# Optimization experiments

Measured on AMD Instinct MI355X. Metric: run time of the kernel, lower is better.

Reference implementation:

```python
import jax, jax.numpy as jnp
import numpy as np

N, NFEAT, NHID, NCLASS, NHEADS = 4096, 512, 64, 40, 8
ALPHA = 0.2  # LeakyReLU negative slope
NEG_BIG = -9e15


def _xavier(key, shape, gain=1.414):
    fan_in, fan_out = shape[0], shape[1]
    bound = gain * np.sqrt(6.0 / (fan_in + fan_out))
    return jax.random.uniform(key, shape, jnp.float32, -bound, bound)


def setup_inputs() -> dict:
    key = jax.random.key(0)
    ks = jax.random.split(key, 6)
    x = jax.random.normal(ks[0], (N, NFEAT), jnp.float32)
    adj = jax.random.randint(ks[1], (N, N), 0, 2).astype(jnp.float32)
    # per-head params of the 8 input GAT layers
    Ws = _xavier(ks[2], (NHEADS, NFEAT, NHID))          # stacked W: [H, F, D]
    a_s = _xavier(ks[3], (NHEADS, 2 * NHID, 1))[..., 0]  # [H, 2D]
    # output GAT layer (concat=False)
    W_out = _xavier(ks[4], (NHID * NHEADS, NCLASS))
    a_out = _xavier(ks[5], (2 * NCLASS, 1))[..., 0]      # [2C]
    return {"x": x, "adj": adj, "Ws": Ws, "a_s": a_s, "W_out": W_out, "a_out": a_out}


def _gat_layer(inp, adj_mask, W, a, concat):
    # h = inp @ W : [N, D]
    h = inp @ W
    D = h.shape[1]
    a1, a2 = a[:D], a[D:]
    # e[i,j] = leakyrelu(a . [h_i, h_j]) = leakyrelu(h_i.a1 + h_j.a2)
    # (same math as the N*N*2D concat in the original, without materializing it)
    f1 = h @ a1  # [N]
    f2 = h @ a2  # [N]
    e = jax.nn.leaky_relu(f1[:, None] + f2[None, :], negative_slope=ALPHA)
    att = jax.nn.softmax(jnp.where(adj_mask, e, NEG_BIG), axis=1)
    h_prime = att @ h  # [N, D]
    return jax.nn.elu(h_prime) if concat else h_prime


def reference(x, adj, Ws, a_s, W_out, a_out):
    adj_mask = adj > 0
    # 8 attention heads over the input features (eval mode: dropout is identity)
    heads = jax.vmap(lambda W, a: _gat_layer(x, adj_mask, W, a, True))(Ws, a_s)  # [H, N, D]
    x2 = jnp.transpose(heads, (1, 0, 2)).reshape(N, NHEADS * NHID)  # concat along feature dim
    out = _gat_layer(x2, adj_mask, W_out, a_out, False)  # [N, C]
    out = jax.nn.elu(out)
    return jax.nn.log_softmax(out, axis=1)
```

## Files before the change

kernel.cpp:

```cpp
#include <hip/hip_runtime.h>
#include <hip/hip_bf16.h>
#include <stdint.h>

#define NN 4096
#define NF 512
#define NH 64
#define NCLS 40
#define NHEADS 8
#define LOG2E 1.4426950408889634f

typedef __attribute__((ext_vector_type(8))) short bh8;
typedef __attribute__((ext_vector_type(4))) float f32x4;

__device__ __forceinline__ unsigned short f2bu(float f) {
    union { float f; unsigned u; } v; v.f = f;
    unsigned r = (v.u + 0x7FFFu + ((v.u >> 16) & 1u)) >> 16;
    return (unsigned short)r;
}
__device__ __forceinline__ float lrelu(float x) { return fmaxf(x, 0.2f * x); }
__device__ __forceinline__ float elu1(float x) { return x > 0.f ? x : expm1f(x); }
__device__ __forceinline__ float exp2fast(float x) {
    float r; asm("v_exp_f32 %0, %1" : "=v"(r) : "v"(x)); return r;
}
__device__ __forceinline__ unsigned fenc(float f) {
    unsigned u = __builtin_bit_cast(unsigned, f);
    return ((int)u < 0) ? ~u : (u | 0x80000000u);
}
__device__ __forceinline__ float fdec(unsigned k) {
    unsigned u = (k & 0x80000000u) ? (k ^ 0x80000000u) : ~k;
    return __builtin_bit_cast(float, u);
}
__device__ __forceinline__ int sbfe1(unsigned v, int off) {
#if __has_builtin(__builtin_amdgcn_sbfe)
    return __builtin_amdgcn_sbfe((int)v, off, 1);
#else
    return ((int)(v << (31 - off))) >> 31;
#endif
}
__device__ __forceinline__ float bmask(float p, unsigned mdw, int bit) {
    return __builtin_bit_cast(float,
        __builtin_bit_cast(unsigned, p) & (unsigned)sbfe1(mdw, bit));
}
__device__ __forceinline__ unsigned pack2(float x, float y) {
    unsigned ux = __builtin_bit_cast(unsigned, x), uy = __builtin_bit_cast(unsigned, y);
    ux += 0x7FFFu + ((ux >> 16) & 1u);
    uy += 0x7FFFu + ((uy >> 16) & 1u);
    return __builtin_amdgcn_perm(uy, ux, 0x07060302u);
}

__global__ __launch_bounds__(256) void prep_all_k(const float* __restrict__ x,
                                                  const float* __restrict__ adj,
                                                  const float* __restrict__ Ws,
                                                  const float* __restrict__ Wo,
                                                  unsigned short* __restrict__ xb,
                                                  unsigned short* __restrict__ WT,
                                                  unsigned short* __restrict__ WoT,
                                                  unsigned char* __restrict__ adjp,
                                                  unsigned* __restrict__ FM1u,
                                                  unsigned* __restrict__ FM2u) {
    const int bid = blockIdx.x, tid = threadIdx.x;
    if (bid < 8192) {
        __shared__ unsigned char sm[4][64];
        const int i = bid >> 1, half = bid & 1;
        const float* rp = adj + (size_t)i * NN + half * 2048 + tid * 8;
        float4 v0 = ((const float4*)rp)[0];
        float4 v1 = ((const float4*)rp)[1];
        unsigned b = (v0.x > 0.f ? 1u : 0u) | (v0.y > 0.f ? 2u : 0u) |
                     (v0.z > 0.f ? 4u : 0u) | (v0.w > 0.f ? 8u : 0u) |
                     (v1.x > 0.f ? 16u : 0u) | (v1.y > 0.f ? 32u : 0u) |
                     (v1.z > 0.f ? 64u : 0u) | (v1.w > 0.f ? 128u : 0u);
        sm[tid & 3][tid >> 2] = (unsigned char)b;
        __syncthreads();
        if (tid < 64) {
            int gp = tid >> 4, word = tid & 15;
            unsigned d = *(const unsigned*)&sm[gp][word * 4];
            *(unsigned*)(adjp + ((size_t)i * 4 + gp) * 128 + half * 64 + word * 4) = d;
        }
    } else if (bid < 10240) {
        if (bid == 8192) {
            if (tid < 8) FM1u[tid] = 0u;
            if (tid == 8) FM2u[0] = 0u;
        }
        int t = (bid - 8192) * 256 + tid;
        float4 v = ((const float4*)x)[t];
        uint2 o; o.x = pack2(v.x, v.y); o.y = pack2(v.z, v.w);
        ((uint2*)xb)[t] = o;
    } else if (bid < 11264) {
        int j = (bid - 10240) * 256 + tid;
        int c = j >> 9, k = j & 511;
        WT[j] = f2bu(Ws[(size_t)(c >> 6) * (NF * NH) + (size_t)k * NH + (c & 63)]);
    } else {
        int j = (bid - 11264) * 256 + tid;
        int c = j >> 9, k = j & 511;
        WoT[j] = f2bu(c < NCLS ? Wo[(size_t)k * NCLS + c] : 0.f);
    }
}

__global__ __launch_bounds__(512) void gemm1_k(const unsigned short* __restrict__ xb,
                                               const unsigned short* __restrict__ WT,
                                               const float* __restrict__ a_s,
                                               unsigned short* __restrict__ Bp1,
                                               float* __restrict__ f1L,
                                               float* __restrict__ f2L,
                                               unsigned* __restrict__ FM1u) {
    __shared__ unsigned short xs[128 * 40];
    __shared__ unsigned short wsm[64 * 40];
    const int tid = threadIdx.x;
    const int w = tid >> 6, lane = tid & 63, r16 = lane & 15, grp = lane >> 4;
    const int i0 = blockIdx.x << 7, h = blockIdx.y, c0 = h << 6;
    const int srow = tid >> 2, sseg = tid & 3;
    const unsigned short* xsrc = xb + (size_t)(i0 + srow) * NF + sseg * 8;
    const unsigned short* wsrc = WT + (size_t)(c0 + (srow & 63)) * NF + sseg * 8;
    f32x4 a0 = {0,0,0,0}, a1 = {0,0,0,0}, a2 = {0,0,0,0}, a3 = {0,0,0,0};
    bh8 rx = *(const bh8*)(xsrc);
    bh8 rw; if (tid < 256) rw = *(const bh8*)(wsrc);
    for (int kb = 0; kb < NF; kb += 32) {
        *(bh8*)(xs + srow * 40 + sseg * 8) = rx;
        if (tid < 256) *(bh8*)(wsm + srow * 40 + sseg * 8) = rw;
        __syncthreads();
        if (kb + 32 < NF) {
            rx = *(const bh8*)(xsrc + kb + 32);
            if (tid < 256) rw = *(const bh8*)(wsrc + kb + 32);
        }
        bh8 af = *(const bh8*)(xs + (w * 16 + r16) * 40 + grp * 8);
        bh8 b0 = *(const bh8*)(wsm + (r16) * 40 + grp * 8);
        bh8 b1 = *(const bh8*)(wsm + (16 + r16) * 40 + grp * 8);
        bh8 b2 = *(const bh8*)(wsm + (32 + r16) * 40 + grp * 8);
        bh8 b3 = *(const bh8*)(wsm + (48 + r16) * 40 + grp * 8);
        a0 = __builtin_amdgcn_mfma_f32_16x16x32_bf16(af, b0, a0, 0, 0, 0);
        a1 = __builtin_amdgcn_mfma_f32_16x16x32_bf16(af, b1, a1, 0, 0, 0);
        a2 = __builtin_amdgcn_mfma_f32_16x16x32_bf16(af, b2, a2, 0, 0, 0);
        a3 = __builtin_amdgcn_mfma_f32_16x16x32_bf16(af, b3, a3, 0, 0, 0);
        __syncthreads();
    }
    const int jt = (i0 >> 5) + (w >> 1);
    const int kg = ((w & 1) << 1) + (grp >> 1);
    const int lanep = kg * 16 + r16;
    const int ebase = (grp & 1) * 4;
    unsigned short* bp = Bp1 + ((size_t)(h * 128 + jt)) * 2048 + lanep * 8 + ebase;
    {
        uint2 v;
        v.x = pack2(a0[0], a0[1]); v.y = pack2(a0[2], a0[3]); *(uint2*)(bp + 0 * 512) = v;
        v.x = pack2(a1[0], a1[1]); v.y = pack2(a1[2], a1[3]); *(uint2*)(bp + 1 * 512) = v;
        v.x = pack2(a2[0], a2[1]); v.y = pack2(a2[2], a2[3]); *(uint2*)(bp + 2 * 512) = v;
        v.x = pack2(a3[0], a3[1]); v.y = pack2(a3[2], a3[3]); *(uint2*)(bp + 3 * 512) = v;
    }
    const float* ap = a_s + h * 128;
    float a1v[4], a2v[4];
#pragma unroll
    for (int n = 0; n < 4; ++n) { a1v[n] = ap[r16 + 16 * n]; a2v[n] = ap[64 + r16 + 16 * n]; }
    float wmax = -3.0e38f;
#pragma unroll
    for (int r = 0; r < 4; ++r) {
        const int orow = i0 + w * 16 + grp * 4 + r;
        float s1 = a0[r] * a1v[0] + a1[r] * a1v[1] + a2[r] * a1v[2] + a3[r] * a1v[3];
        float s2 = a0[r] * a2v[0] + a1[r] * a2v[1] + a2[r] * a2v[2] + a3[r] * a2v[3];
#pragma unroll
        for (int o2 = 1; o2 < 16; o2 <<= 1) { s1 += __shfl_xor(s1, o2); s2 += __shfl_xor(s2, o2); }
        s1 *= LOG2E; s2 *= LOG2E;
        if (r16 == 0) { f1L[h * NN + orow] = s1; f2L[h * NN + orow] = s2; }
        wmax = fmaxf(wmax, s2);
    }
    wmax = fmaxf(wmax, __shfl_xor(wmax, 16));
    wmax = fmaxf(wmax, __shfl_xor(wmax, 32));
    if (lane == 0) atomicMax(&FM1u[h], fenc(wmax));
}

__global__ __launch_bounds__(256) void gemm2_k(const unsigned short* __restrict__ x2b,
                                               const unsigned short* __restrict__ WoT,
                                               const float* __restrict__ a_out,
                                               unsigned short* __restrict__ Bp2,
                                               float* __restrict__ f12L,
                                               float* __restrict__ f22L,
                                               unsigned* __restrict__ FM2u) {
    __shared__ unsigned short xs[64 * 40];
    __shared__ unsigned short wsm[48 * 40];
    const int tid = threadIdx.x;
    const int w = tid >> 6, lane = tid & 63, r16 = lane & 15, grp = lane >> 4;
    const int i0 = blockIdx.x << 6;
    const int srow = tid >> 2, sseg = tid & 3;
    const unsigned short* xsrc = x2b + (size_t)(i0 + srow) * NF + sseg * 8;
    const unsigned short* wsrc = WoT + (size_t)srow * NF + sseg * 8;
    f32x4 a0 = {0,0,0,0}, a1 = {0,0,0,0}, a2 = {0,0,0,0};
    bh8 rx = *(const bh8*)(xsrc);
    bh8 rw; if (tid < 192) rw = *(const bh8*)(wsrc);
    for (int kb = 0; kb < NF; kb += 32) {
        *(bh8*)(xs + srow * 40 + sseg * 8) = rx;
        if (tid < 192) *(bh8*)(wsm + srow * 40 + sseg * 8) = rw;
        __syncthreads();
        if (kb + 32 < NF) {
            rx = *(const bh8*)(xsrc + kb + 32);
            if (tid < 192) rw = *(const bh8*)(wsrc + kb + 32);
        }
        bh8 af = *(const bh8*)(xs + (w * 16 + r16) * 40 + grp * 8);
        bh8 b0 = *(const bh8*)(wsm + (r16) * 40 + grp * 8);
        bh8 b1 = *(const bh8*)(wsm + (16 + r16) * 40 + grp * 8);
        bh8 b2 = *(const bh8*)(wsm + (32 + r16) * 40 + grp * 8);
        a0 = __builtin_amdgcn_mfma_f32_16x16x32_bf16(af, b0, a0, 0, 0, 0);
        a1 = __builtin_amdgcn_mfma_f32_16x16x32_bf16(af, b1, a1, 0, 0, 0);
        a2 = __builtin_amdgcn_mfma_f32_16x16x32_bf16(af, b2, a2, 0, 0, 0);
        __syncthreads();
    }
    const int jt = (i0 >> 5) + (w >> 1);
    const int kg = ((w & 1) << 1) + (grp >> 1);
    const int lanep = kg * 16 + r16;
    const int ebase = (grp & 1) * 4;
    unsigned short* bp = Bp2 + (size_t)jt * 1536 + lanep * 8 + ebase;
    {
        uint2 v;
        v.x = pack2(a0[0], a0[1]); v.y = pack2(a0[2], a0[3]); *(uint2*)(bp + 0 * 512) = v;
        v.x = pack2(a1[0], a1[1]); v.y = pack2(a1[2], a1[3]); *(uint2*)(bp + 1 * 512) = v;
        v.x = pack2(a2[0], a2[1]); v.y = pack2(a2[2], a2[3]); *(uint2*)(bp + 2 * 512) = v;
    }
    float a1v[3], a2v[3];
#pragma unroll
    for (int n = 0; n < 3; ++n) {
        int col = r16 + 16 * n;
        a1v[n] = col < NCLS ? a_out[col] : 0.f;
        a2v[n] = col < NCLS ? a_out[NCLS + col] : 0.f;
    }
    float wmax = -3.0e38f;
#pragma unroll
    for (int r = 0; r < 4; ++r) {
        const int orow = i0 + w * 16 + grp * 4 + r;
        float s1 = a0[r] * a1v[0] + a1[r] * a1v[1] + a2[r] * a1v[2];
        float s2 = a0[r] * a2v[0] + a1[r] * a2v[1] + a2[r] * a2v[2];
#pragma unroll
        for (int o2 = 1; o2 < 16; o2 <<= 1) { s1 += __shfl_xor(s1, o2); s2 += __shfl_xor(s2, o2); }
        s1 *= LOG2E; s2 *= LOG2E;
        if (r16 == 0) { f12L[orow] = s1; f22L[orow] = s2; }
        wmax = fmaxf(wmax, s2);
    }
    wmax = fmaxf(wmax, __shfl_xor(wmax, 16));
    wmax = fmaxf(wmax, __shfl_xor(wmax, 32));
    if (lane == 0) atomicMax(&FM2u[0], fenc(wmax));
}

__global__ __launch_bounds__(512, 6) void attn1_k(const unsigned short* __restrict__ Bp1,
                                                  const unsigned char* __restrict__ adjp,
                                                  const float* __restrict__ f1L,
                                                  const float* __restrict__ f2L,
                                                  const unsigned* __restrict__ FM1u,
                                                  unsigned short* __restrict__ x2b) {
    __shared__ float EFs[8192];
    const int tid = threadIdx.x, w = tid >> 6, lane = tid & 63;
    const int r16 = lane & 15, grp = lane >> 4;
    const int rowg = w & 3, jq = w >> 2;
    const int h = blockIdx.y;
    const int i0 = blockIdx.x * 64;
    const float fm = fdec(FM1u[h]);
    const float* f2p = f2L + h * NN;
    for (int t = 0; t < 8; ++t) {
        int j = tid + t * 512;
        float d = f2p[j] - fm;
        EFs[2 * j] = exp2fast(d);
        EFs[2 * j + 1] = exp2fast(0.2f * d);
    }
    const int irow = i0 + rowg * 16 + r16;
    const float f1v = f1L[h * NN + irow];
    const float mL = lrelu(f1v + fm);
    const float A = exp2fast(f1v + fm - mL);
    const float B = exp2fast(__builtin_fmaf(0.2f, f1v + fm, -mL));
    __syncthreads();
    const int jtbase = jq * 64;
    const unsigned char* adjr = adjp + ((size_t)irow * 4 + grp) * 128 + jtbase;
    const float* efp = EFs + grp * 16;
    const unsigned short* Bbase = Bp1 + (size_t)h * 128 * 2048 + lane * 8;
    f32x4 acc0 = {0,0,0,0}, acc1 = {0,0,0,0}, acc2 = {0,0,0,0}, acc3 = {0,0,0,0}, accd = {0,0,0,0};
    const short ov = (r16 == 0) ? (short)0x3F80 : (short)0;
    bh8 ones;
#pragma unroll
    for (int e = 0; e < 8; ++e) ones[e] = ov;
    bh8 nb0, nb1, nb2, nb3;
#define PREF1(JT) { const unsigned short* Bn = Bbase + (size_t)(JT) * 2048;              \
        nb0 = *(const bh8*)(Bn);        nb1 = *(const bh8*)(Bn + 512);                    \
        nb2 = *(const bh8*)(Bn + 1024); nb3 = *(const bh8*)(Bn + 1536); }
    PREF1(jtbase);
    for (int jt16 = 0; jt16 < 4; ++jt16) {
        const uint4 a4 = *(const uint4*)(adjr + jt16 * 16);
#pragma unroll
        for (int q = 0; q < 4; ++q) {
            const unsigned mdw = (q == 0) ? a4.x : (q == 1) ? a4.y : (q == 2) ? a4.z : a4.w;
#pragma unroll
            for (int u = 0; u < 4; ++u) {
                const int jt = jtbase + jt16 * 16 + q * 4 + u;
                bh8 b0 = nb0, b1 = nb1, b2 = nb2, b3 = nb3;
                PREF1(jt + 1);
                const float* e4 = efp + jt * 64;
                float4 ea = *(const float4*)(e4);
                float4 eb = *(const float4*)(e4 + 4);
                float4 ec = *(const float4*)(e4 + 8);
                float4 ed = *(const float4*)(e4 + 12);
                const int bb = u * 8;
                union { bh8 v; unsigned u32[4]; } pk;
                {
                    float p0 = bmask(fmaxf(A * ea.x, B * ea.y), mdw, bb + 0);
                    float p1 = bmask(fmaxf(A * ea.z, B * ea.w), mdw, bb + 1);
                    pk.u32[0] = __builtin_amdgcn_perm(__builtin_bit_cast(unsigned, p1),
                                                      __builtin_bit_cast(unsigned, p0), 0x07060302u);
                    float p2 = bmask(fmaxf(A * eb.x, B * eb.y), mdw, bb + 2);
                    float p3 = bmask(fmaxf(A * eb.z, B * eb.w), mdw, bb + 3);
                    pk.u32[1] = __builtin_amdgcn_perm(__builtin_bit_cast(unsigned, p3),
                                                      __builtin_bit_cast(unsigned, p2), 0x07060302u);
                    float p4 = bmask(fmaxf(A * ec.x, B * ec.y), mdw, bb + 4);
                    float p5 = bmask(fmaxf(A * ec.z, B * ec.w), mdw, bb + 5);
                    pk.u32[2] = __builtin_amdgcn_perm(__builtin_bit_cast(unsigned, p5),
                                                      __builtin_bit_cast(unsigned, p4), 0x07060302u);
                    float p6 = bmask(fmaxf(A * ed.x, B * ed.y), mdw, bb + 6);
                    float p7 = bmask(fmaxf(A * ed.z, B * ed.w), mdw, bb + 7);
                    pk.u32[3] = __builtin_amdgcn_perm(__builtin_bit_cast(unsigned, p7),
                                                      __builtin_bit_cast(unsigned, p6), 0x07060302u);
                }
                acc0 = __builtin_amdgcn_mfma_f32_16x16x32_bf16(pk.v, b0, acc0, 0, 0, 0);
                acc1 = __builtin_amdgcn_mfma_f32_16x16x32_bf16(pk.v, b1, acc1, 0, 0, 0);
                acc2 = __builtin_amdgcn_mfma_f32_16x16x32_bf16(pk.v, b2, acc2, 0, 0, 0);
                acc3 = __builtin_amdgcn_mfma_f32_16x16x32_bf16(pk.v, b3, acc3, 0, 0, 0);
                accd = __builtin_amdgcn_mfma_f32_16x16x32_bf16(pk.v, ones, accd, 0, 0, 0);
            }
        }
    }
#undef PREF1
    __syncthreads();
    float (*comb)[64][21] = (float(*)[64][21])EFs;
    if (jq == 1) {
        float* cb = &comb[rowg][lane][0];
#pragma unroll
        for (int r = 0; r < 4; ++r) {
            cb[r] = acc0[r]; cb[4 + r] = acc1[r]; cb[8 + r] = acc2[r];
            cb[12 + r] = acc3[r]; cb[16 + r] = accd[r];
        }
    }
    __syncthreads();
    if (jq == 0) {
        const float* cb = &comb[rowg][lane][0];
#pragma unroll
        for (int r = 0; r < 4; ++r) {
            acc0[r] += cb[r]; acc1[r] += cb[4 + r]; acc2[r] += cb[8 + r];
            acc3[r] += cb[12 + r]; accd[r] += cb[16 + r];
        }
#pragma unroll
        for (int r = 0; r < 4; ++r) {
            const float den = __shfl(accd[r], lane & 48);
            const float inv = 1.0f / den;
            unsigned short* o = x2b + (size_t)(i0 + rowg * 16 + grp * 4 + r) * NF + h * 64 + r16;
            o[0]  = f2bu(elu1(acc0[r] * inv));
            o[16] = f2bu(elu1(acc1[r] * inv));
            o[32] = f2bu(elu1(acc2[r] * inv));
            o[48] = f2bu(elu1(acc3[r] * inv));
        }
    }
}

__global__ __launch_bounds__(512, 6) void attn2_k(const unsigned short* __restrict__ Bp2,
                                                  const unsigned char* __restrict__ adjp,
                                                  const float* __restrict__ f12L,
                                                  const float* __restrict__ f22L,
                                                  const unsigned* __restrict__ FM2u,
                                                  float* __restrict__ out) {
    __shared__ float EFs[8192];
    __shared__ float comb[8][64][17];
    const int tid = threadIdx.x, w = tid >> 6, lane = tid & 63;
    const int r16 = lane & 15, grp = lane >> 4;
    const int i0 = blockIdx.x * 16;
    const int i = i0 + r16;
    const float fm = fdec(FM2u[0]);
    for (int t = 0; t < 8; ++t) {
        int j = tid + t * 512;
        float d = f22L[j] - fm;
        EFs[2 * j] = exp2fast(d);
        EFs[2 * j + 1] = exp2fast(0.2f * d);
    }
    const float f1v = f12L[i];
    const float mL = lrelu(f1v + fm);
    const float A = exp2fast(f1v + fm - mL);
    const float B = exp2fast(__builtin_fmaf(0.2f, f1v + fm, -mL));
    __syncthreads();
    const int jt0 = w * 16;
    const uint4 a4 = *(const uint4*)(adjp + ((size_t)i * 4 + grp) * 128 + jt0);
    f32x4 acc0 = {0,0,0,0}, acc1 = {0,0,0,0}, acc2 = {0,0,0,0}, accd = {0,0,0,0};
    const short ov = (r16 == 0) ? (short)0x3F80 : (short)0;
    bh8 ones;
#pragma unroll
    for (int e = 0; e < 8; ++e) ones[e] = ov;
    const unsigned short* Bbase = Bp2 + lane * 8;
    const float* efp = EFs + grp * 16;
    bh8 nb0, nb1, nb2;
#define PREF2(JT) { const unsigned short* Bn = Bbase + (size_t)(JT) * 1536;              \
        nb0 = *(const bh8*)(Bn); nb1 = *(const bh8*)(Bn + 512); nb2 = *(const bh8*)(Bn + 1024); }
    PREF2(jt0);
#pragma unroll
    for (int q = 0; q < 4; ++q) {
        const unsigned mdw = (q == 0) ? a4.x : (q == 1) ? a4.y : (q == 2) ? a4.z : a4.w;
#pragma unroll
        for (int u = 0; u < 4; ++u) {
            const int jt = jt0 + q * 4 + u;
            bh8 b0 = nb0, b1 = nb1, b2 = nb2;
            PREF2(jt + 1);
            const float* e4 = efp + jt * 64;
            float4 ea = *(const float4*)(e4);
            float4 eb = *(const float4*)(e4 + 4);
            float4 ec = *(const float4*)(e4 + 8);
            float4 ed = *(const float4*)(e4 + 12);
            const int bb = u * 8;
            union { bh8 v; unsigned u32[4]; } pk;
            {
                float p0 = bmask(fmaxf(A * ea.x, B * ea.y), mdw, bb + 0);
                float p1 = bmask(fmaxf(A * ea.z, B * ea.w), mdw, bb + 1);
                pk.u32[0] = __builtin_amdgcn_perm(__builtin_bit_cast(unsigned, p1),
                                                  __builtin_bit_cast(unsigned, p0), 0x07060302u);
                float p2 = bmask(fmaxf(A * eb.x, B * eb.y), mdw, bb + 2);
                float p3 = bmask(fmaxf(A * eb.z, B * eb.w), mdw, bb + 3);
                pk.u32[1] = __builtin_amdgcn_perm(__builtin_bit_cast(unsigned, p3),
                                                  __builtin_bit_cast(unsigned, p2), 0x07060302u);
                float p4 = bmask(fmaxf(A * ec.x, B * ec.y), mdw, bb + 4);
                float p5 = bmask(fmaxf(A * ec.z, B * ec.w), mdw, bb + 5);
                pk.u32[2] = __builtin_amdgcn_perm(__builtin_bit_cast(unsigned, p5),
                                                  __builtin_bit_cast(unsigned, p4), 0x07060302u);
                float p6 = bmask(fmaxf(A * ed.x, B * ed.y), mdw, bb + 6);
                float p7 = bmask(fmaxf(A * ed.z, B * ed.w), mdw, bb + 7);
                pk.u32[3] = __builtin_amdgcn_perm(__builtin_bit_cast(unsigned, p7),
                                                  __builtin_bit_cast(unsigned, p6), 0x07060302u);
            }
            acc0 = __builtin_amdgcn_mfma_f32_16x16x32_bf16(pk.v, b0, acc0, 0, 0, 0);
            acc1 = __builtin_amdgcn_mfma_f32_16x16x32_bf16(pk.v, b1, acc1, 0, 0, 0);
            acc2 = __builtin_amdgcn_mfma_f32_16x16x32_bf16(pk.v, b2, acc2, 0, 0, 0);
            accd = __builtin_amdgcn_mfma_f32_16x16x32_bf16(pk.v, ones, accd, 0, 0, 0);
        }
    }
#undef PREF2
    {
        float* cb = &comb[w][lane][0];
#pragma unroll
        for (int r = 0; r < 4; ++r) {
            cb[r] = acc0[r]; cb[4 + r] = acc1[r]; cb[8 + r] = acc2[r]; cb[12 + r] = accd[r];
        }
    }
    __syncthreads();
    if (w < 4) {
        const float* sb = &comb[w + 4][lane][0];
        float* cb = &comb[w][lane][0];
#pragma unroll
        for (int r = 0; r < 4; ++r) {
            acc0[r] += sb[r]; acc1[r] += sb[4 + r]; acc2[r] += sb[8 + r]; accd[r] += sb[12 + r];
            cb[r] = acc0[r]; cb[4 + r] = acc1[r]; cb[8 + r] = acc2[r]; cb[12 + r] = accd[r];
        }
    }
    __syncthreads();
    if (w < 2) {
        const float* sb = &comb[w + 2][lane][0];
        float* cb = &comb[w][lane][0];
#pragma unroll
        for (int r = 0; r < 4; ++r) {
            acc0[r] += sb[r]; acc1[r] += sb[4 + r]; acc2[r] += sb[8 + r]; accd[r] += sb[12 + r];
            cb[r] = acc0[r]; cb[4 + r] = acc1[r]; cb[8 + r] = acc2[r]; cb[12 + r] = accd[r];
        }
    }
    __syncthreads();
    if (w == 0) {
        const float* sb = &comb[1][lane][0];
#pragma unroll
        for (int r = 0; r < 4; ++r) {
            acc0[r] += sb[r]; acc1[r] += sb[4 + r]; acc2[r] += sb[8 + r]; accd[r] += sb[12 + r];
        }
#pragma unroll
        for (int r = 0; r < 4; ++r) {
            const int row = grp * 4 + r;
            const float den = __shfl(accd[r], lane & 48);
            const float inv = 1.0f / den;
            float v0 = elu1(acc0[r] * inv);
            float v1 = elu1(acc1[r] * inv);
            float v2 = (r16 < 8) ? elu1(acc2[r] * inv) : -3.0e38f;
            float mx = fmaxf(fmaxf(v0, v1), v2);
#pragma unroll
            for (int o = 1; o < 16; o <<= 1) mx = fmaxf(mx, __shfl_xor(mx, o));
            float ex = __expf(v0 - mx) + __expf(v1 - mx) + ((r16 < 8) ? __expf(v2 - mx) : 0.f);
#pragma unroll
            for (int o = 1; o < 16; o <<= 1) ex += __shfl_xor(ex, o);
            const float lse = mx + logf(ex);
            float* op = out + (size_t)(i0 + row) * NCLS;
            op[r16] = v0 - lse;
            op[16 + r16] = v1 - lse;
            if (r16 < 8) op[32 + r16] = v2 - lse;
        }
    }
}

#define OFF_XB   0ULL
#define OFF_WT   4194304ULL
#define OFF_WOT  4718592ULL
#define OFF_BP1  4767744ULL
#define OFF_X2B  8962048ULL
#define OFF_BP2  13156352ULL
#define OFF_F1L  13549568ULL
#define OFF_F2L  13680640ULL
#define OFF_F12  13811712ULL
#define OFF_F22  13828096ULL
#define OFF_FM1  13844480ULL
#define OFF_FM2  13844736ULL
#define OFF_ADJ  13844992ULL

extern "C" void kernel_launch(void* const* d_in, const int* in_sizes, int n_in,
                              void* d_out, int out_size, void* d_ws, size_t ws_size,
                              hipStream_t stream) {
    const float* x     = (const float*)d_in[0];
    const float* adj   = (const float*)d_in[1];
    const float* Ws    = (const float*)d_in[2];
    const float* a_s   = (const float*)d_in[3];
    const float* W_out = (const float*)d_in[4];
    const float* a_out = (const float*)d_in[5];
    float* out = (float*)d_out;
    char* w = (char*)d_ws;

    unsigned short* xb  = (unsigned short*)(w + OFF_XB);
    unsigned short* WT  = (unsigned short*)(w + OFF_WT);
    unsigned short* WoT = (unsigned short*)(w + OFF_WOT);
    unsigned short* Bp1 = (unsigned short*)(w + OFF_BP1);
    unsigned short* x2b = (unsigned short*)(w + OFF_X2B);
    unsigned short* Bp2 = (unsigned short*)(w + OFF_BP2);
    float* f1L = (float*)(w + OFF_F1L);
    float* f2L = (float*)(w + OFF_F2L);
    float* f12 = (float*)(w + OFF_F12);
    float* f22 = (float*)(w + OFF_F22);
    unsigned* FM1u = (unsigned*)(w + OFF_FM1);
    unsigned* FM2u = (unsigned*)(w + OFF_FM2);
    unsigned char* adjp = (unsigned char*)(w + OFF_ADJ);

    prep_all_k<<<11360, 256, 0, stream>>>(x, adj, Ws, W_out, xb, WT, WoT, adjp, FM1u, FM2u);
    gemm1_k<<<dim3(32, 8), 512, 0, stream>>>(xb, WT, a_s, Bp1, f1L, f2L, FM1u);
    attn1_k<<<dim3(64, 8), 512, 0, stream>>>(Bp1, adjp, f1L, f2L, FM1u, x2b);
    gemm2_k<<<64, 256, 0, stream>>>(x2b, WoT, a_out, Bp2, f12, f22, FM2u);
    attn2_k<<<256, 512, 0, stream>>>(Bp2, adjp, f12, f22, FM2u, out);
}
```

Baseline: 207.3 us.

## Tile packed adjacency bitmask by 64-row block for coalesced mask loads

The packed adjacency bitmask is stored in a new layout grouped by 64-row block and by 32-column dword index, with row and lane-group innermost. Each mask dword load in the attention kernels is then coalesced across the wavefront instead of strided per row. attn1 replaces its per-16-tile uint4 load with a software-prefetched dword load one step ahead, and attn2 issues its mask loads before the softmax-table setup. The trade is more, smaller load instructions and a scattered write pattern in the prep kernel.

```diff
diff --git a/kernel.cpp b/kernel.cpp
--- a/kernel.cpp
+++ b/kernel.cpp
@@ -55,7 +55,7 @@
                                                   unsigned short* __restrict__ xb,
                                                   unsigned short* __restrict__ WT,
                                                   unsigned short* __restrict__ WoT,
-                                                  unsigned char* __restrict__ adjp,
+                                                  unsigned* __restrict__ adjq,
                                                   unsigned* __restrict__ FM1u,
                                                   unsigned* __restrict__ FM2u) {
     const int bid = blockIdx.x, tid = threadIdx.x;
@@ -74,7 +74,8 @@
         if (tid < 64) {
             int gp = tid >> 4, word = tid & 15;
             unsigned d = *(const unsigned*)&sm[gp][word * 4];
-            *(unsigned*)(adjp + ((size_t)i * 4 + gp) * 128 + half * 64 + word * 4) = d;
+            int ib = i >> 6, row = i & 63, jt4 = half * 16 + word;
+            adjq[(size_t)ib * 8192 + (size_t)jt4 * 256 + row * 4 + gp] = d;
         }
     } else if (bid < 10240) {
         if (bid == 8192) {
@@ -237,7 +238,7 @@
 }
 
 __global__ __launch_bounds__(512, 6) void attn1_k(const unsigned short* __restrict__ Bp1,
-                                                  const unsigned char* __restrict__ adjp,
+                                                  const unsigned* __restrict__ adjq,
                                                   const float* __restrict__ f1L,
                                                   const float* __restrict__ f2L,
                                                   const unsigned* __restrict__ FM1u,
@@ -263,7 +264,7 @@
     const float B = exp2fast(__builtin_fmaf(0.2f, f1v + fm, -mL));
     __syncthreads();
     const int jtbase = jq * 64;
-    const unsigned char* adjr = adjp + ((size_t)irow * 4 + grp) * 128 + jtbase;
+    const unsigned* adjl = adjq + (size_t)blockIdx.x * 8192 + (rowg * 16 + r16) * 4 + grp;
     const float* efp = EFs + grp * 16;
     const unsigned short* Bbase = Bp1 + (size_t)h * 128 * 2048 + lane * 8;
     f32x4 acc0 = {0,0,0,0}, acc1 = {0,0,0,0}, acc2 = {0,0,0,0}, acc3 = {0,0,0,0}, accd = {0,0,0,0};
@@ -276,47 +277,46 @@
         nb0 = *(const bh8*)(Bn);        nb1 = *(const bh8*)(Bn + 512);                    \
         nb2 = *(const bh8*)(Bn + 1024); nb3 = *(const bh8*)(Bn + 1536); }
     PREF1(jtbase);
-    for (int jt16 = 0; jt16 < 4; ++jt16) {
-        const uint4 a4 = *(const uint4*)(adjr + jt16 * 16);
-#pragma unroll
-        for (int q = 0; q < 4; ++q) {
-            const unsigned mdw = (q == 0) ? a4.x : (q == 1) ? a4.y : (q == 2) ? a4.z : a4.w;
-#pragma unroll
-            for (int u = 0; u < 4; ++u) {
-                const int jt = jtbase + jt16 * 16 + q * 4 + u;
-                bh8 b0 = nb0, b1 = nb1, b2 = nb2, b3 = nb3;
-                PREF1(jt + 1);
-                const float* e4 = efp + jt * 64;
-                float4 ea = *(const float4*)(e4);
-                float4 eb = *(const float4*)(e4 + 4);
-                float4 ec = *(const float4*)(e4 + 8);
-                float4 ed = *(const float4*)(e4 + 12);
-                const int bb = u * 8;
-                union { bh8 v; unsigned u32[4]; } pk;
-                {
-                    float p0 = bmask(fmaxf(A * ea.x, B * ea.y), mdw, bb + 0);
-                    float p1 = bmask(fmaxf(A * ea.z, B * ea.w), mdw, bb + 1);
-                    pk.u32[0] = __builtin_amdgcn_perm(__builtin_bit_cast(unsigned, p1),
-                                                      __builtin_bit_cast(unsigned, p0), 0x07060302u);
-                    float p2 = bmask(fmaxf(A * eb.x, B * eb.y), mdw, bb + 2);
-                    float p3 = bmask(fmaxf(A * eb.z, B * eb.w), mdw, bb + 3);
-                    pk.u32[1] = __builtin_amdgcn_perm(__builtin_bit_cast(unsigned, p3),
-                                                      __builtin_bit_cast(unsigned, p2), 0x07060302u);
-                    float p4 = bmask(fmaxf(A * ec.x, B * ec.y), mdw, bb + 4);
-                    float p5 = bmask(fmaxf(A * ec.z, B * ec.w), mdw, bb + 5);
-                    pk.u32[2] = __builtin_amdgcn_perm(__builtin_bit_cast(unsigned, p5),
-                                                      __builtin_bit_cast(unsigned, p4), 0x07060302u);
-                    float p6 = bmask(fmaxf(A * ed.x, B * ed.y), mdw, bb + 6);
-                    float p7 = bmask(fmaxf(A * ed.z, B * ed.w), mdw, bb + 7);
-                    pk.u32[3] = __builtin_amdgcn_perm(__builtin_bit_cast(unsigned, p7),
-                                                      __builtin_bit_cast(unsigned, p6), 0x07060302u);
-                }
-                acc0 = __builtin_amdgcn_mfma_f32_16x16x32_bf16(pk.v, b0, acc0, 0, 0, 0);
-                acc1 = __builtin_amdgcn_mfma_f32_16x16x32_bf16(pk.v, b1, acc1, 0, 0, 0);
-                acc2 = __builtin_amdgcn_mfma_f32_16x16x32_bf16(pk.v, b2, acc2, 0, 0, 0);
-                acc3 = __builtin_amdgcn_mfma_f32_16x16x32_bf16(pk.v, b3, acc3, 0, 0, 0);
-                accd = __builtin_amdgcn_mfma_f32_16x16x32_bf16(pk.v, ones, accd, 0, 0, 0);
+    unsigned nmdw = adjl[(size_t)(jq * 16) * 256];
+    for (int jt4i = 0; jt4i < 16; ++jt4i) {
+        const int jt4 = jq * 16 + jt4i;
+        const unsigned mdw = nmdw;
+        if (jt4i < 15) nmdw = adjl[(size_t)(jt4 + 1) * 256];
+#pragma unroll
+        for (int u = 0; u < 4; ++u) {
+            const int jt = jt4 * 4 + u;
+            bh8 b0 = nb0, b1 = nb1, b2 = nb2, b3 = nb3;
+            PREF1(jt + 1);
+            const float* e4 = efp + jt * 64;
+            float4 ea = *(const float4*)(e4);
+            float4 eb = *(const float4*)(e4 + 4);
+            float4 ec = *(const float4*)(e4 + 8);
+            float4 ed = *(const float4*)(e4 + 12);
+            const int bb = u * 8;
+            union { bh8 v; unsigned u32[4]; } pk;
+            {
+                float p0 = bmask(fmaxf(A * ea.x, B * ea.y), mdw, bb + 0);
+                float p1 = bmask(fmaxf(A * ea.z, B * ea.w), mdw, bb + 1);
+                pk.u32[0] = __builtin_amdgcn_perm(__builtin_bit_cast(unsigned, p1),
+                                                  __builtin_bit_cast(unsigned, p0), 0x07060302u);
+                float p2 = bmask(fmaxf(A * eb.x, B * eb.y), mdw, bb + 2);
+                float p3 = bmask(fmaxf(A * eb.z, B * eb.w), mdw, bb + 3);
+                pk.u32[1] = __builtin_amdgcn_perm(__builtin_bit_cast(unsigned, p3),
+                                                  __builtin_bit_cast(unsigned, p2), 0x07060302u);
+                float p4 = bmask(fmaxf(A * ec.x, B * ec.y), mdw, bb + 4);
+                float p5 = bmask(fmaxf(A * ec.z, B * ec.w), mdw, bb + 5);
+                pk.u32[2] = __builtin_amdgcn_perm(__builtin_bit_cast(unsigned, p5),
+                                                  __builtin_bit_cast(unsigned, p4), 0x07060302u);
+                float p6 = bmask(fmaxf(A * ed.x, B * ed.y), mdw, bb + 6);
+                float p7 = bmask(fmaxf(A * ed.z, B * ed.w), mdw, bb + 7);
+                pk.u32[3] = __builtin_amdgcn_perm(__builtin_bit_cast(unsigned, p7),
+                                                  __builtin_bit_cast(unsigned, p6), 0x07060302u);
             }
+            acc0 = __builtin_amdgcn_mfma_f32_16x16x32_bf16(pk.v, b0, acc0, 0, 0, 0);
+            acc1 = __builtin_amdgcn_mfma_f32_16x16x32_bf16(pk.v, b1, acc1, 0, 0, 0);
+            acc2 = __builtin_amdgcn_mfma_f32_16x16x32_bf16(pk.v, b2, acc2, 0, 0, 0);
+            acc3 = __builtin_amdgcn_mfma_f32_16x16x32_bf16(pk.v, b3, acc3, 0, 0, 0);
+            accd = __builtin_amdgcn_mfma_f32_16x16x32_bf16(pk.v, ones, accd, 0, 0, 0);
         }
     }
 #undef PREF1
@@ -352,7 +352,7 @@
 }
 
 __global__ __launch_bounds__(512, 6) void attn2_k(const unsigned short* __restrict__ Bp2,
-                                                  const unsigned char* __restrict__ adjp,
+                                                  const unsigned* __restrict__ adjq,
                                                   const float* __restrict__ f12L,
                                                   const float* __restrict__ f22L,
                                                   const unsigned* __restrict__ FM2u,
@@ -363,6 +363,11 @@
     const int r16 = lane & 15, grp = lane >> 4;
     const int i0 = blockIdx.x * 16;
     const int i = i0 + r16;
+    const unsigned* adjl = adjq + (size_t)(i0 >> 6) * 8192 + ((i0 & 63) + r16) * 4 + grp;
+    unsigned m0 = adjl[(size_t)(w * 4 + 0) * 256];
+    unsigned m1 = adjl[(size_t)(w * 4 + 1) * 256];
+    unsigned m2 = adjl[(size_t)(w * 4 + 2) * 256];
+    unsigned m3 = adjl[(size_t)(w * 4 + 3) * 256];
     const float fm = fdec(FM2u[0]);
     for (int t = 0; t < 8; ++t) {
         int j = tid + t * 512;
@@ -376,7 +381,6 @@
     const float B = exp2fast(__builtin_fmaf(0.2f, f1v + fm, -mL));
     __syncthreads();
     const int jt0 = w * 16;
-    const uint4 a4 = *(const uint4*)(adjp + ((size_t)i * 4 + grp) * 128 + jt0);
     f32x4 acc0 = {0,0,0,0}, acc1 = {0,0,0,0}, acc2 = {0,0,0,0}, accd = {0,0,0,0};
     const short ov = (r16 == 0) ? (short)0x3F80 : (short)0;
     bh8 ones;
@@ -390,7 +394,7 @@
     PREF2(jt0);
 #pragma unroll
     for (int q = 0; q < 4; ++q) {
-        const unsigned mdw = (q == 0) ? a4.x : (q == 1) ? a4.y : (q == 2) ? a4.z : a4.w;
+        const unsigned mdw = (q == 0) ? m0 : (q == 1) ? m1 : (q == 2) ? m2 : m3;
 #pragma unroll
         for (int u = 0; u < 4; ++u) {
             const int jt = jt0 + q * 4 + u;
@@ -523,11 +527,11 @@
     float* f22 = (float*)(w + OFF_F22);
     unsigned* FM1u = (unsigned*)(w + OFF_FM1);
     unsigned* FM2u = (unsigned*)(w + OFF_FM2);
-    unsigned char* adjp = (unsigned char*)(w + OFF_ADJ);
-
-    prep_all_k<<<11360, 256, 0, stream>>>(x, adj, Ws, W_out, xb, WT, WoT, adjp, FM1u, FM2u);
+    unsigned* adjq = (unsigned*)(w + OFF_ADJ);
+
+    prep_all_k<<<11360, 256, 0, stream>>>(x, adj, Ws, W_out, xb, WT, WoT, adjq, FM1u, FM2u);
     gemm1_k<<<dim3(32, 8), 512, 0, stream>>>(xb, WT, a_s, Bp1, f1L, f2L, FM1u);
-    attn1_k<<<dim3(64, 8), 512, 0, stream>>>(Bp1, adjp, f1L, f2L, FM1u, x2b);
+    attn1_k<<<dim3(64, 8), 512, 0, stream>>>(Bp1, adjq, f1L, f2L, FM1u, x2b);
     gemm2_k<<<64, 256, 0, stream>>>(x2b, WoT, a_out, Bp2, f12, f22, FM2u);
-    attn2_k<<<256, 512, 0, stream>>>(Bp2, adjp, f12, f22, FM2u, out);
-}
+    attn2_k<<<256, 512, 0, stream>>>(Bp2, adjq, f12, f22, FM2u, out);
+}
```

Measured after the change: 271.8 us. 31.1% more time.

## Stage adjacency tile in LDS and compute exp tables in two halves

Applied to the files above, without the earlier changes.

The attention kernel now copies the block's 64-row adjacency bitmask into padded shared memory, and each warp reads its mask words from LDS with a one-step prefetch. The per-column exponent table is built in two halves of 2048 columns rather than all at once, which frees shared memory to hold the mask. Each half gets its own barrier, and the warp split across columns changes to match. This aims to take strided global adjacency loads off the inner loop and keep the LDS footprint in check, at the cost of an extra sync and a serialized table build between halves.

```diff
diff --git a/kernel.cpp b/kernel.cpp
--- a/kernel.cpp
+++ b/kernel.cpp
@@ -242,7 +242,8 @@
                                                   const float* __restrict__ f2L,
                                                   const unsigned* __restrict__ FM1u,
                                                   unsigned short* __restrict__ x2b) {
-    __shared__ float EFs[8192];
+    __shared__ float SH[12544];
+    unsigned* ADJd = (unsigned*)&SH[4096];
     const int tid = threadIdx.x, w = tid >> 6, lane = tid & 63;
     const int r16 = lane & 15, grp = lane >> 4;
     const int rowg = w & 3, jq = w >> 2;
@@ -250,21 +251,19 @@
     const int i0 = blockIdx.x * 64;
     const float fm = fdec(FM1u[h]);
     const float* f2p = f2L + h * NN;
-    for (int t = 0; t < 8; ++t) {
-        int j = tid + t * 512;
-        float d = f2p[j] - fm;
-        EFs[2 * j] = exp2fast(d);
-        EFs[2 * j + 1] = exp2fast(0.2f * d);
+    {
+        const unsigned* asrc = (const unsigned*)(adjp + (size_t)i0 * 512);
+        for (int t = 0; t < 16; ++t) {
+            int idx = tid + t * 512;
+            ADJd[(idx >> 5) * 33 + (idx & 31)] = asrc[idx];
+        }
     }
     const int irow = i0 + rowg * 16 + r16;
     const float f1v = f1L[h * NN + irow];
     const float mL = lrelu(f1v + fm);
     const float A = exp2fast(f1v + fm - mL);
     const float B = exp2fast(__builtin_fmaf(0.2f, f1v + fm, -mL));
-    __syncthreads();
-    const int jtbase = jq * 64;
-    const unsigned char* adjr = adjp + ((size_t)irow * 4 + grp) * 128 + jtbase;
-    const float* efp = EFs + grp * 16;
+    const unsigned* adjl = ADJd + ((rowg * 16 + r16) * 4 + grp) * 33;
     const unsigned short* Bbase = Bp1 + (size_t)h * 128 * 2048 + lane * 8;
     f32x4 acc0 = {0,0,0,0}, acc1 = {0,0,0,0}, acc2 = {0,0,0,0}, acc3 = {0,0,0,0}, accd = {0,0,0,0};
     const short ov = (r16 == 0) ? (short)0x3F80 : (short)0;
@@ -275,18 +274,27 @@
 #define PREF1(JT) { const unsigned short* Bn = Bbase + (size_t)(JT) * 2048;              \
         nb0 = *(const bh8*)(Bn);        nb1 = *(const bh8*)(Bn + 512);                    \
         nb2 = *(const bh8*)(Bn + 1024); nb3 = *(const bh8*)(Bn + 1536); }
-    PREF1(jtbase);
-    for (int jt16 = 0; jt16 < 4; ++jt16) {
-        const uint4 a4 = *(const uint4*)(adjr + jt16 * 16);
-#pragma unroll
-        for (int q = 0; q < 4; ++q) {
-            const unsigned mdw = (q == 0) ? a4.x : (q == 1) ? a4.y : (q == 2) ? a4.z : a4.w;
+    for (int half = 0; half < 2; ++half) {
+        for (int t = 0; t < 4; ++t) {
+            int jl = tid + t * 512;
+            float d = f2p[half * 2048 + jl] - fm;
+            SH[2 * jl] = exp2fast(d);
+            SH[2 * jl + 1] = exp2fast(0.2f * d);
+        }
+        __syncthreads();
+        const int jt4l0 = jq * 8;
+        PREF1(half * 64 + jt4l0 * 4);
+        unsigned nmdw = adjl[half * 16 + jt4l0];
+        for (int jt4i = 0; jt4i < 8; ++jt4i) {
+            const int jt4l = jt4l0 + jt4i;
+            const unsigned mdw = nmdw;
+            if (jt4i < 7) nmdw = adjl[half * 16 + jt4l + 1];
 #pragma unroll
             for (int u = 0; u < 4; ++u) {
-                const int jt = jtbase + jt16 * 16 + q * 4 + u;
+                const int jtl = jt4l * 4 + u;
                 bh8 b0 = nb0, b1 = nb1, b2 = nb2, b3 = nb3;
-                PREF1(jt + 1);
-                const float* e4 = efp + jt * 64;
+                PREF1(half * 64 + jtl + 1);
+                const float* e4 = SH + jtl * 64 + grp * 16;
                 float4 ea = *(const float4*)(e4);
                 float4 eb = *(const float4*)(e4 + 4);
                 float4 ec = *(const float4*)(e4 + 8);
@@ -318,10 +326,10 @@
                 accd = __builtin_amdgcn_mfma_f32_16x16x32_bf16(pk.v, ones, accd, 0, 0, 0);
             }
         }
+        __syncthreads();
     }
 #undef PREF1
-    __syncthreads();
-    float (*comb)[64][21] = (float(*)[64][21])EFs;
+    float (*comb)[64][21] = (float(*)[64][21])SH;
     if (jq == 1) {
         float* cb = &comb[rowg][lane][0];
 #pragma unroll
```

After: 251.5 us. +21.3%, slower.
